# Kernel tuning notes

Hardware: AMD Instinct MI355X
Metric: run time of the kernel (lower is better)

Reference implementation:

```python
import jax, jax.numpy as jnp
import numpy as np

B, C, N, K = 8, 256, 1024, 16
CQ = C // 4
EPS_BN = 1e-5

def setup_inputs() -> dict:
    key = jax.random.key(0)
    ks = jax.random.split(key, 8)
    s = lambda fan: 1.0 / np.sqrt(fan)
    return {
        "x": jax.random.normal(ks[0], (B, C, N, K), dtype=jnp.float32),
        "q_w": jax.random.normal(ks[1], (CQ, C), dtype=jnp.float32) * s(C),
        "k_w": jax.random.normal(ks[2], (CQ, C), dtype=jnp.float32) * s(C),
        "v_w": jax.random.normal(ks[3], (C, C), dtype=jnp.float32) * s(C),
        "v_b": jax.random.normal(ks[4], (C,), dtype=jnp.float32) * 0.01,
        "t_w": jax.random.normal(ks[5], (C, C), dtype=jnp.float32) * s(C),
        "t_b": jax.random.normal(ks[6], (C,), dtype=jnp.float32) * 0.01,
        "gamma": jnp.ones((C,), dtype=jnp.float32),
        "beta": jnp.zeros((C,), dtype=jnp.float32),
    }

def reference(x, q_w, k_w, v_w, v_b, t_w, t_b, gamma, beta):
    # 1x1 convs == channel matmuls
    xq = jnp.einsum('bcnk,oc->bonk', x, q_w)                  # [B,CQ,N,K]
    xk = jnp.einsum('bcnk,oc->bonk', x, k_w)                  # [B,CQ,N,K]
    xv = jnp.einsum('bcnk,oc->bonk', x, v_w) + v_b[None, :, None, None]  # [B,C,N,K]
    x_q = jnp.transpose(xq, (0, 3, 2, 1))                     # [B,K,N,CQ]
    x_k = jnp.transpose(xk, (0, 3, 1, 2))                     # [B,K,CQ,N]
    x_v = jnp.transpose(xv, (0, 3, 1, 2))                     # [B,K,C,N]
    energy = jnp.einsum('bknd,bkdm->bknm', x_q, x_k)          # [B,K,N,N]
    attn = jax.nn.softmax(energy, axis=-1)
    # non-standard renormalization across the K (neighbourhood) axis
    attn = attn / (1e-9 + jnp.sum(attn, axis=1, keepdims=True))
    x_r = jnp.einsum('bkcn,bknm->bkcm', x_v, attn)            # [B,K,C,N]
    x_r = jnp.transpose(x_r, (0, 2, 3, 1))                    # [B,C,N,K]
    d = x - x_r
    t = jnp.einsum('bcnk,oc->bonk', d, t_w) + t_b[None, :, None, None]
    # BatchNorm2d (training-mode batch statistics, biased variance)
    mean = jnp.mean(t, axis=(0, 2, 3), keepdims=True)
    var = jnp.mean((t - mean) ** 2, axis=(0, 2, 3), keepdims=True)
    t_hat = (t - mean) / jnp.sqrt(var + EPS_BN)
    r = jax.nn.relu(t_hat * gamma[None, :, None, None] + beta[None, :, None, None])
    return x + r
```

## Files before the change

kernel.cpp:

```cpp
#include <hip/hip_runtime.h>
#include <hip/hip_bf16.h>
#include <cstdint>
#include <cstddef>

#define NB   8
#define NCHN 256
#define NSP  1024
#define NKK  16
#define NCQ  64
#define NPK  16384
#define NBK  128

typedef __hip_bfloat16 bf16;
typedef unsigned short u16;
typedef __attribute__((ext_vector_type(8))) short bf16x8;
typedef __attribute__((ext_vector_type(4))) float f32x4;

__device__ __forceinline__ float bf2f(bf16 v) { return __bfloat162float(v); }

__device__ __forceinline__ u16 f2bf(float x) {
  unsigned b = __float_as_uint(x);
  return (u16)((b + 0x7FFF + ((b >> 16) & 1)) >> 16);
}
__device__ __forceinline__ float bfr2f(u16 u) { return __uint_as_float(((unsigned)u) << 16); }

__device__ __forceinline__ void stage64(const u16* __restrict__ g, u16* __restrict__ l, int t) {
  #pragma unroll
  for (int i = 0; i < 2; ++i) {
    const int idx = t + i * 256;
    const int row = idx >> 3, col = (idx & 7) * 8;
    const bf16x8 v = *reinterpret_cast<const bf16x8*>(g + (size_t)row * 64 + col);
    *reinterpret_cast<bf16x8*>(l + row * 72 + col) = v;
  }
}

__global__ __launch_bounds__(256) void k_w2(const float* __restrict__ t_w,
                                            const float* __restrict__ v_w,
                                            const float* __restrict__ v_b,
                                            float* __restrict__ w2,
                                            float* __restrict__ ub) {
  const int o = blockIdx.x;
  const int c = threadIdx.x;
  __shared__ float trow[NCHN];
  __shared__ float red[NCHN];
  trow[c] = t_w[o * NCHN + c];
  __syncthreads();
  float acc = 0.f;
  for (int m = 0; m < NCHN; ++m) acc = fmaf(trow[m], v_w[m * NCHN + c], acc);
  w2[o * NCHN + c] = acc;
  red[c] = trow[c] * v_b[c];
  __syncthreads();
  for (int s = 128; s > 0; s >>= 1) {
    if (c < s) red[c] += red[c + s];
    __syncthreads();
  }
  if (c == 0) ub[o] = red[0];
}

__global__ __launch_bounds__(256) void k_wsplit(
    const float* __restrict__ q_w, const float* __restrict__ k_w,
    const float* __restrict__ w2, const float* __restrict__ t_w,
    u16* __restrict__ wh, u16* __restrict__ wl) {
  const int o = blockIdx.x, c = threadIdx.x;
  float v;
  if (o < 64)       v = q_w[o * NCHN + c];
  else if (o < 128) v = k_w[(o - 64) * NCHN + c];
  else if (o < 384) v = w2[(o - 128) * NCHN + c];
  else              v = t_w[(o - 384) * NCHN + c];
  const u16 hi = f2bf(v);
  wh[o * NCHN + c] = hi;
  wl[o * NCHN + c] = f2bf(v - bfr2f(hi));
}

__global__ __launch_bounds__(256) void k_xsplit(
    const float* __restrict__ x, u16* __restrict__ xh, u16* __restrict__ xl) {
  const int c0 = blockIdx.x * 64, p0 = blockIdx.y * 64, b = blockIdx.z;
  const int t = threadIdx.x;
  __shared__ float tile[64][65];
  const float* xb = x + ((size_t)b * NCHN + c0) * NPK + p0;
  #pragma unroll
  for (int it = 0; it < 4; ++it) {
    const int item = t + it * 256;
    const int row = item >> 4, colg = item & 15;
    const float4 v = *reinterpret_cast<const float4*>(xb + (size_t)row * NPK + colg * 4);
    tile[row][colg * 4 + 0] = v.x;
    tile[row][colg * 4 + 1] = v.y;
    tile[row][colg * 4 + 2] = v.z;
    tile[row][colg * 4 + 3] = v.w;
  }
  __syncthreads();
  #pragma unroll
  for (int it = 0; it < 2; ++it) {
    const int item = t + it * 256;
    const int pl = item >> 3, cg = item & 7;
    u16 hi[8], lo[8];
    #pragma unroll
    for (int jj = 0; jj < 8; ++jj) {
      const float v = tile[cg * 8 + jj][pl];
      hi[jj] = f2bf(v);
      lo[jj] = f2bf(v - bfr2f(hi[jj]));
    }
    const int p = p0 + pl;
    const int pp = (p & 15) * NSP + (p >> 4);
    const size_t base = ((size_t)b * NPK + pp) * NCHN + c0 + cg * 8;
    *reinterpret_cast<bf16x8*>(xh + base) = *reinterpret_cast<const bf16x8*>(hi);
    *reinterpret_cast<bf16x8*>(xl + base) = *reinterpret_cast<const bf16x8*>(lo);
  }
}

__global__ void k_zero(float* __restrict__ p, int n) {
  int i = blockIdx.x * 256 + threadIdx.x;
  if (i < n) p[i] = 0.f;
}

__global__ __launch_bounds__(256) void k_projm(
    const u16* __restrict__ xh, const u16* __restrict__ xl,
    const u16* __restrict__ wh, const u16* __restrict__ wl,
    const float* __restrict__ ub,
    u16* __restrict__ qh, u16* __restrict__ ql,
    u16* __restrict__ kh, u16* __restrict__ kl,
    u16* __restrict__ u, u16* __restrict__ s) {
  const int oh = blockIdx.x;
  const int p0 = blockIdx.y * 64;
  const int kk = p0 >> 10;
  const int n0 = p0 & 1023;
  const int b  = blockIdx.z;
  const int t = threadIdx.x, w = t >> 6, lane = t & 63, l15 = lane & 15, quad = lane >> 4;
  const int obase = oh * 320 + w * 80;
  const bool anyqk = obase < 128;
  __shared__ u16 lxh[64 * 264];
  __shared__ u16 lxl[64 * 264];
  const u16* xhb = xh + ((size_t)b * NPK + p0) * NCHN;
  const u16* xlb = xl + ((size_t)b * NPK + p0) * NCHN;
  #pragma unroll
  for (int i = 0; i < 8; ++i) {
    const int idx = t + i * 256;
    const int row = idx >> 5, col8 = (idx & 31) * 8;
    *reinterpret_cast<bf16x8*>(&lxh[row * 264 + col8]) =
        *reinterpret_cast<const bf16x8*>(xhb + (size_t)row * NCHN + col8);
  }
  if (oh == 0) {
    #pragma unroll
    for (int i = 0; i < 8; ++i) {
      const int idx = t + i * 256;
      const int row = idx >> 5, col8 = (idx & 31) * 8;
      *reinterpret_cast<bf16x8*>(&lxl[row * 264 + col8]) =
          *reinterpret_cast<const bf16x8*>(xlb + (size_t)row * NCHN + col8);
    }
  }
  __syncthreads();
  f32x4 acc[5][4] = {};
  for (int kc = 0; kc < 8; ++kc) {
    const int c0 = kc * 32 + quad * 8;
    bf16x8 bhf[4], blf[4];
    #pragma unroll
    for (int fj = 0; fj < 4; ++fj) {
      bhf[fj] = *reinterpret_cast<const bf16x8*>(&lxh[(fj * 16 + l15) * 264 + c0]);
      if (anyqk) blf[fj] = *reinterpret_cast<const bf16x8*>(&lxl[(fj * 16 + l15) * 264 + c0]);
    }
    #pragma unroll
    for (int fi = 0; fi < 5; ++fi) {
      const int orow = obase + fi * 16;
      const size_t aoff = (size_t)(orow + l15) * NCHN + c0;
      const bf16x8 ah = *reinterpret_cast<const bf16x8*>(wh + aoff);
      if (orow < 128) {
        const bf16x8 al = *reinterpret_cast<const bf16x8*>(wl + aoff);
        #pragma unroll
        for (int fj = 0; fj < 4; ++fj) {
          acc[fi][fj] = __builtin_amdgcn_mfma_f32_16x16x32_bf16(ah, bhf[fj], acc[fi][fj], 0, 0, 0);
          acc[fi][fj] = __builtin_amdgcn_mfma_f32_16x16x32_bf16(ah, blf[fj], acc[fi][fj], 0, 0, 0);
          acc[fi][fj] = __builtin_amdgcn_mfma_f32_16x16x32_bf16(al, bhf[fj], acc[fi][fj], 0, 0, 0);
        }
      } else {
        #pragma unroll
        for (int fj = 0; fj < 4; ++fj)
          acc[fi][fj] = __builtin_amdgcn_mfma_f32_16x16x32_bf16(bhf[fj], ah, acc[fi][fj], 0, 0, 0);
      }
    }
  }
  #pragma unroll
  for (int fi = 0; fi < 5; ++fi) {
    const int orow = obase + fi * 16;
    if (orow < 128) {
      const int ob = orow + quad * 4;
      #pragma unroll
      for (int fj = 0; fj < 4; ++fj) {
        const int n = n0 + fj * 16 + l15;
        ushort4 hv, lv;
        #pragma unroll
        for (int r = 0; r < 4; ++r) {
          const float v = acc[fi][fj][r];
          const u16 hi = f2bf(v);
          ((u16*)&hv)[r] = hi;
          ((u16*)&lv)[r] = f2bf(v - bfr2f(hi));
        }
        const size_t rowb = ((size_t)(b * NKK + kk) * NSP + n) * NCQ;
        if (ob < 64) {
          *reinterpret_cast<ushort4*>(qh + rowb + ob) = hv;
          *reinterpret_cast<ushort4*>(ql + rowb + ob) = lv;
        } else {
          *reinterpret_cast<ushort4*>(kh + rowb + (ob - 64)) = hv;
          *reinterpret_cast<ushort4*>(kl + rowb + (ob - 64)) = lv;
        }
      }
    } else if (orow < 384) {
      const int c = orow + l15 - 128;
      const float uc = ub[c];
      u16* up = u + ((size_t)(b * NKK + kk) * NCHN + c) * NSP;
      #pragma unroll
      for (int fj = 0; fj < 4; ++fj) {
        const int n = n0 + fj * 16 + quad * 4;
        ushort4 uv;
        #pragma unroll
        for (int r = 0; r < 4; ++r) ((u16*)&uv)[r] = f2bf(acc[fi][fj][r] + uc);
        *reinterpret_cast<ushort4*>(up + n) = uv;
      }
    } else {
      const int c = orow + l15 - 384;
      u16* sp = s + (((size_t)b * NCHN + c) * NKK + kk) * NSP;
      #pragma unroll
      for (int fj = 0; fj < 4; ++fj) {
        const int n = n0 + fj * 16 + quad * 4;
        ushort4 sv;
        #pragma unroll
        for (int r = 0; r < 4; ++r) ((u16*)&sv)[r] = f2bf(acc[fi][fj][r]);
        *reinterpret_cast<ushort4*>(sp + n) = sv;
      }
    }
  }
}

__global__ __launch_bounds__(256) void k_stats(
    const u16* __restrict__ qh_g, const u16* __restrict__ ql_g,
    const u16* __restrict__ kh_g, const u16* __restrict__ kl_g,
    float* __restrict__ m_i, float* __restrict__ inv_l) {
  const int n0 = blockIdx.x * 64;
  const int bk = blockIdx.y;
  const int t = threadIdx.x;
  const int w = t >> 6, lane = t & 63, l15 = lane & 15, quad = lane >> 4;
  __shared__ u16 sqh[64 * 72], sql[64 * 72], skh[64 * 72], skl[64 * 72];
  const size_t qoff = (size_t)bk * NSP * NCQ + (size_t)n0 * NCQ;
  stage64(qh_g + qoff, sqh, t);
  stage64(ql_g + qoff, sql, t);
  float runmax[4] = {-1e30f, -1e30f, -1e30f, -1e30f};
  float runsum[4] = {0.f, 0.f, 0.f, 0.f};
  const int arow = w * 16 + l15;
  for (int mt = 0; mt < 16; ++mt) {
    __syncthreads();
    const size_t koff = (size_t)bk * NSP * NCQ + (size_t)(mt * 64) * NCQ;
    stage64(kh_g + koff, skh, t);
    stage64(kl_g + koff, skl, t);
    __syncthreads();
    f32x4 e[4] = {};
    #pragma unroll
    for (int ks = 0; ks < 2; ++ks) {
      const bf16x8 ah = *(const bf16x8*)&sqh[arow * 72 + ks * 32 + quad * 8];
      const bf16x8 al = *(const bf16x8*)&sql[arow * 72 + ks * 32 + quad * 8];
      #pragma unroll
      for (int fj = 0; fj < 4; ++fj) {
        const int brow = fj * 16 + l15;
        const bf16x8 bh = *(const bf16x8*)&skh[brow * 72 + ks * 32 + quad * 8];
        const bf16x8 bl = *(const bf16x8*)&skl[brow * 72 + ks * 32 + quad * 8];
        e[fj] = __builtin_amdgcn_mfma_f32_16x16x32_bf16(ah, bh, e[fj], 0, 0, 0);
        e[fj] = __builtin_amdgcn_mfma_f32_16x16x32_bf16(ah, bl, e[fj], 0, 0, 0);
        e[fj] = __builtin_amdgcn_mfma_f32_16x16x32_bf16(al, bh, e[fj], 0, 0, 0);
      }
    }
    #pragma unroll
    for (int r = 0; r < 4; ++r) {
      float tmax = fmaxf(fmaxf(e[0][r], e[1][r]), fmaxf(e[2][r], e[3][r]));
      tmax = fmaxf(tmax, __shfl_xor(tmax, 1));
      tmax = fmaxf(tmax, __shfl_xor(tmax, 2));
      tmax = fmaxf(tmax, __shfl_xor(tmax, 4));
      tmax = fmaxf(tmax, __shfl_xor(tmax, 8));
      const float nm = fmaxf(runmax[r], tmax);
      float ts = __expf(e[0][r] - nm) + __expf(e[1][r] - nm) +
                 __expf(e[2][r] - nm) + __expf(e[3][r] - nm);
      ts += __shfl_xor(ts, 1);
      ts += __shfl_xor(ts, 2);
      ts += __shfl_xor(ts, 4);
      ts += __shfl_xor(ts, 8);
      runsum[r] = runsum[r] * __expf(runmax[r] - nm) + ts;
      runmax[r] = nm;
    }
  }
  if (l15 == 0) {
    #pragma unroll
    for (int r = 0; r < 4; ++r) {
      const int n = n0 + w * 16 + quad * 4 + r;
      m_i[(size_t)bk * NSP + n] = runmax[r];
      inv_l[(size_t)bk * NSP + n] = 1.0f / runsum[r];
    }
  }
}

__global__ __launch_bounds__(256) void k_denom(
    const u16* __restrict__ qh_g, const u16* __restrict__ ql_g,
    const u16* __restrict__ kh_g, const u16* __restrict__ kl_g,
    const float* __restrict__ m_i, const float* __restrict__ inv_l,
    float* __restrict__ invden) {
  const int m0 = blockIdx.x * 64, n0 = blockIdx.y * 64, b = blockIdx.z;
  const int t = threadIdx.x;
  const int w = t >> 6, lane = t & 63, l15 = lane & 15, quad = lane >> 4;
  __shared__ u16 sqh[64 * 72], sql[64 * 72], skh[64 * 72], skl[64 * 72];
  float den[4][4] = {};
  const int arow = w * 16 + l15;
  for (int kk = 0; kk < NKK; ++kk) {
    const int bk = b * NKK + kk;
    __syncthreads();
    const size_t qoff = (size_t)bk * NSP * NCQ + (size_t)n0 * NCQ;
    const size_t koff = (size_t)bk * NSP * NCQ + (size_t)m0 * NCQ;
    stage64(qh_g + qoff, sqh, t);
    stage64(ql_g + qoff, sql, t);
    stage64(kh_g + koff, skh, t);
    stage64(kl_g + koff, skl, t);
    __syncthreads();
    f32x4 e[4] = {};
    #pragma unroll
    for (int ks = 0; ks < 2; ++ks) {
      const bf16x8 ah = *(const bf16x8*)&sqh[arow * 72 + ks * 32 + quad * 8];
      const bf16x8 al = *(const bf16x8*)&sql[arow * 72 + ks * 32 + quad * 8];
      #pragma unroll
      for (int fj = 0; fj < 4; ++fj) {
        const int brow = fj * 16 + l15;
        const bf16x8 bh = *(const bf16x8*)&skh[brow * 72 + ks * 32 + quad * 8];
        const bf16x8 bl = *(const bf16x8*)&skl[brow * 72 + ks * 32 + quad * 8];
        e[fj] = __builtin_amdgcn_mfma_f32_16x16x32_bf16(ah, bh, e[fj], 0, 0, 0);
        e[fj] = __builtin_amdgcn_mfma_f32_16x16x32_bf16(ah, bl, e[fj], 0, 0, 0);
        e[fj] = __builtin_amdgcn_mfma_f32_16x16x32_bf16(al, bh, e[fj], 0, 0, 0);
      }
    }
    float smv[4], slv[4];
    #pragma unroll
    for (int r = 0; r < 4; ++r) {
      const int n = n0 + w * 16 + quad * 4 + r;
      smv[r] = m_i[(size_t)bk * NSP + n];
      slv[r] = inv_l[(size_t)bk * NSP + n];
    }
    #pragma unroll
    for (int fj = 0; fj < 4; ++fj)
      #pragma unroll
      for (int r = 0; r < 4; ++r)
        den[fj][r] += __expf(e[fj][r] - smv[r]) * slv[r];
  }
  #pragma unroll
  for (int fj = 0; fj < 4; ++fj)
    #pragma unroll
    for (int r = 0; r < 4; ++r) {
      const int n = n0 + w * 16 + quad * 4 + r;
      invden[(size_t)b * NSP * NSP + (size_t)n * NSP + m0 + fj * 16 + l15] =
          1.0f / (1e-9f + den[fj][r]);
    }
}

__global__ __launch_bounds__(256) void k_xr(
    const u16* __restrict__ qh_g, const u16* __restrict__ ql_g,
    const u16* __restrict__ kh_g, const u16* __restrict__ kl_g,
    const u16* __restrict__ u_g, const float* __restrict__ m_i,
    const float* __restrict__ inv_l, const float* __restrict__ invden,
    u16* __restrict__ txr) {
  const int m0 = blockIdx.x * 64;
  const int bk = blockIdx.y;
  const int b = bk >> 4;
  const int t = threadIdx.x;
  const int w = t >> 6, lane = t & 63, l15 = lane & 15, quad = lane >> 4;
  __shared__ u16 sqh[64 * 72], sql[64 * 72], skh[64 * 72], skl[64 * 72];
  __shared__ u16 sat[64 * 72];
  f32x4 acc[4][4] = {};
  const size_t koff = (size_t)bk * NSP * NCQ + (size_t)m0 * NCQ;
  stage64(kh_g + koff, skh, t);
  stage64(kl_g + koff, skl, t);
  const float* dp = invden + (size_t)b * NSP * NSP;
  const u16* up = u_g + (size_t)bk * NCHN * NSP;
  const int arow = w * 16 + l15;
  for (int nt = 0; nt < 16; ++nt) {
    const int n0 = nt * 64;
    __syncthreads();
    const size_t qoff = (size_t)bk * NSP * NCQ + (size_t)n0 * NCQ;
    stage64(qh_g + qoff, sqh, t);
    stage64(ql_g + qoff, sql, t);
    __syncthreads();
    f32x4 e[4] = {};
    #pragma unroll
    for (int ks = 0; ks < 2; ++ks) {
      const bf16x8 ah = *(const bf16x8*)&sqh[arow * 72 + ks * 32 + quad * 8];
      const bf16x8 al = *(const bf16x8*)&sql[arow * 72 + ks * 32 + quad * 8];
      #pragma unroll
      for (int fj = 0; fj < 4; ++fj) {
        const int brow = fj * 16 + l15;
        const bf16x8 bh = *(const bf16x8*)&skh[brow * 72 + ks * 32 + quad * 8];
        const bf16x8 bl = *(const bf16x8*)&skl[brow * 72 + ks * 32 + quad * 8];
        e[fj] = __builtin_amdgcn_mfma_f32_16x16x32_bf16(ah, bh, e[fj], 0, 0, 0);
        e[fj] = __builtin_amdgcn_mfma_f32_16x16x32_bf16(ah, bl, e[fj], 0, 0, 0);
        e[fj] = __builtin_amdgcn_mfma_f32_16x16x32_bf16(al, bh, e[fj], 0, 0, 0);
      }
    }
    float smv[4], slv[4];
    #pragma unroll
    for (int r = 0; r < 4; ++r) {
      const int n = n0 + w * 16 + quad * 4 + r;
      smv[r] = m_i[(size_t)bk * NSP + n];
      slv[r] = inv_l[(size_t)bk * NSP + n];
    }
    #pragma unroll
    for (int fj = 0; fj < 4; ++fj) {
      const int m = m0 + fj * 16 + l15;
      float p[4];
      #pragma unroll
      for (int r = 0; r < 4; ++r) {
        const int n = n0 + w * 16 + quad * 4 + r;
        p[r] = __expf(e[fj][r] - smv[r]) * slv[r] * dp[(size_t)n * NSP + m];
      }
      ushort4 pk;
      pk.x = f2bf(p[0]); pk.y = f2bf(p[1]); pk.z = f2bf(p[2]); pk.w = f2bf(p[3]);
      *reinterpret_cast<ushort4*>(&sat[(fj * 16 + l15) * 72 + w * 16 + quad * 4]) = pk;
    }
    __syncthreads();
    #pragma unroll
    for (int ks = 0; ks < 2; ++ks) {
      bf16x8 bfr[4];
      #pragma unroll
      for (int fj = 0; fj < 4; ++fj)
        bfr[fj] = *(const bf16x8*)&sat[(fj * 16 + l15) * 72 + ks * 32 + quad * 8];
      #pragma unroll
      for (int ci = 0; ci < 4; ++ci) {
        const int c = w * 64 + ci * 16 + l15;
        const bf16x8 a =
            *reinterpret_cast<const bf16x8*>(up + (size_t)c * NSP + n0 + ks * 32 + quad * 8);
        #pragma unroll
        for (int fj = 0; fj < 4; ++fj)
          acc[ci][fj] = __builtin_amdgcn_mfma_f32_16x16x32_bf16(a, bfr[fj], acc[ci][fj], 0, 0, 0);
      }
    }
  }
  #pragma unroll
  for (int ci = 0; ci < 4; ++ci)
    #pragma unroll
    for (int fj = 0; fj < 4; ++fj)
      #pragma unroll
      for (int r = 0; r < 4; ++r) {
        const int c = w * 64 + ci * 16 + quad * 4 + r;
        const int m = m0 + fj * 16 + l15;
        txr[((size_t)bk * NCHN + c) * NSP + m] = f2bf(acc[ci][fj][r]);
      }
}

__global__ __launch_bounds__(256) void k_bnstats(
    const u16* __restrict__ s, const u16* __restrict__ txr,
    const float* __restrict__ t_b, float* __restrict__ bnsum,
    float* __restrict__ bnsq) {
  const int c = blockIdx.x, b = blockIdx.y, t = threadIdx.x;
  __shared__ float r1[256], r2[256];
  const u16* sp = s + (size_t)(b * NCHN + c) * NKK * NSP;
  const u16* tp = txr + ((size_t)b * NKK * NCHN + c) * NSP;
  const float tb = t_b[c];
  float lsum = 0.f, lss = 0.f;
  #pragma unroll
  for (int it = 0; it < 8; ++it) {
    const int idx = (it * 256 + t) * 8;
    const int kk = idx >> 10, n = idx & 1023;
    const bf16x8 s8 = *reinterpret_cast<const bf16x8*>(sp + idx);
    const bf16x8 t8 = *reinterpret_cast<const bf16x8*>(tp + (size_t)kk * NCHN * NSP + n);
    #pragma unroll
    for (int j = 0; j < 8; ++j) {
      const float tv = bfr2f((u16)s8[j]) + tb - bfr2f((u16)t8[j]);
      lsum += tv;
      lss = fmaf(tv, tv, lss);
    }
  }
  r1[t] = lsum; r2[t] = lss;
  __syncthreads();
  for (int sh = 128; sh > 0; sh >>= 1) {
    if (t < sh) { r1[t] += r1[t + sh]; r2[t] += r2[t + sh]; }
    __syncthreads();
  }
  if (t == 0) {
    atomicAdd(&bnsum[c], r1[0]);
    atomicAdd(&bnsq[c], r2[0]);
  }
}

__global__ void k_bnfin(const float* __restrict__ bnsum, const float* __restrict__ bnsq,
                        const float* __restrict__ gamma, const float* __restrict__ beta,
                        float* __restrict__ abuf, float* __restrict__ bbuf) {
  const int c = threadIdx.x;
  const float inv_m = 1.0f / 131072.0f;
  const float mean = bnsum[c] * inv_m;
  const float var = bnsq[c] * inv_m - mean * mean;
  const float a = gamma[c] * rsqrtf(var + 1e-5f);
  abuf[c] = a;
  bbuf[c] = beta[c] - mean * a;
}

__global__ __launch_bounds__(256) void k_out(
    const float* __restrict__ x, const u16* __restrict__ s,
    const u16* __restrict__ txr, const float* __restrict__ t_b,
    const float* __restrict__ abuf, const float* __restrict__ bbuf,
    float* __restrict__ out) {
  const int c = blockIdx.x, b = blockIdx.y, t = threadIdx.x;
  __shared__ u16 txl[16 * 264];
  __shared__ u16 sxl[16 * 264];
  const u16* sp = s + (size_t)(b * NCHN + c) * NKK * NSP;
  const u16* tp = txr + ((size_t)b * NKK * NCHN + c) * NSP;
  const float* xp = x + ((size_t)b * NCHN + c) * NPK;
  float* op = out + ((size_t)b * NCHN + c) * NPK;
  const float tb = t_b[c], a = abuf[c], bb = bbuf[c];
  for (int n0 = 0; n0 < NSP; n0 += 256) {
    __syncthreads();
    #pragma unroll
    for (int it = 0; it < 2; ++it) {
      const int item = it * 256 + t;
      const int kk = item >> 5, nn8 = (item & 31) * 8;
      *reinterpret_cast<bf16x8*>(&txl[kk * 264 + nn8]) =
          *reinterpret_cast<const bf16x8*>(tp + (size_t)kk * NCHN * NSP + n0 + nn8);
      *reinterpret_cast<bf16x8*>(&sxl[kk * 264 + nn8]) =
          *reinterpret_cast<const bf16x8*>(sp + (size_t)kk * NSP + n0 + nn8);
    }
    __syncthreads();
    for (int i2 = t; i2 < 1024; i2 += 256) {
      const int idx = i2 * 4;
      const int nn = idx >> 4, k0 = idx & 15;
      const float4 xv = *reinterpret_cast<const float4*>(xp + (size_t)n0 * NKK + idx);
      float4 ov;
      float* ovp = &ov.x;
      const float* xvp = &xv.x;
      #pragma unroll
      for (int j = 0; j < 4; ++j) {
        const int kk = k0 + j;
        const float tv = bfr2f(sxl[kk * 264 + nn]) + tb - bfr2f(txl[kk * 264 + nn]);
        ovp[j] = xvp[j] + fmaxf(fmaf(tv, a, bb), 0.f);
      }
      *reinterpret_cast<float4*>(op + (size_t)n0 * NKK + idx) = ov;
    }
  }
}

extern "C" void kernel_launch(void* const* d_in, const int* in_sizes, int n_in,
                              void* d_out, int out_size, void* d_ws, size_t ws_size,
                              hipStream_t stream) {
  (void)in_sizes; (void)n_in; (void)out_size; (void)ws_size;
  const float* x     = (const float*)d_in[0];
  const float* q_w   = (const float*)d_in[1];
  const float* k_w   = (const float*)d_in[2];
  const float* v_w   = (const float*)d_in[3];
  const float* v_b   = (const float*)d_in[4];
  const float* t_w   = (const float*)d_in[5];
  const float* t_b   = (const float*)d_in[6];
  const float* gamma = (const float*)d_in[7];
  const float* beta  = (const float*)d_in[8];
  float* out = (float*)d_out;

  char* w = (char*)d_ws;
  float* invden = (float*)w; w += (size_t)NB * NSP * NSP * 4;
  u16*   txr    = (u16*)w;   w += (size_t)NBK * NCHN * NSP * 2;
  u16*   qh     = (u16*)w;   w += (size_t)NBK * NSP * NCQ * 2;
  u16*   ql     = (u16*)w;   w += (size_t)NBK * NSP * NCQ * 2;
  u16*   kh     = (u16*)w;   w += (size_t)NBK * NSP * NCQ * 2;
  u16*   kl     = (u16*)w;   w += (size_t)NBK * NSP * NCQ * 2;
  u16*   u      = (u16*)w;   w += (size_t)NBK * NCHN * NSP * 2;
  u16*   s      = (u16*)w;   w += (size_t)NB * NCHN * NPK * 2;
  u16*   xh     = (u16*)w;   w += (size_t)NB * NPK * NCHN * 2;
  u16*   xl     = (u16*)w;   w += (size_t)NB * NPK * NCHN * 2;
  u16*   whb    = (u16*)w;   w += (size_t)640 * NCHN * 2;
  u16*   wlb    = (u16*)w;   w += (size_t)640 * NCHN * 2;
  float* m_i    = (float*)w; w += (size_t)NBK * NSP * 4;
  float* inv_l  = (float*)w; w += (size_t)NBK * NSP * 4;
  float* w2     = (float*)w; w += (size_t)NCHN * NCHN * 4;
  float* ub     = (float*)w; w += 1024;
  float* bnsum  = (float*)w; w += 1024;
  float* bnsq   = (float*)w; w += 1024;
  float* abuf   = (float*)w; w += 1024;
  float* bbuf   = (float*)w; w += 1024;

  k_zero<<<dim3(2), dim3(256), 0, stream>>>(bnsum, 512);
  k_w2<<<dim3(256), dim3(256), 0, stream>>>(t_w, v_w, v_b, w2, ub);
  k_wsplit<<<dim3(640), dim3(256), 0, stream>>>(q_w, k_w, w2, t_w, whb, wlb);
  k_xsplit<<<dim3(4, 256, NB), dim3(256), 0, stream>>>(x, xh, xl);
  k_projm<<<dim3(2, 256, NB), dim3(256), 0, stream>>>(xh, xl, whb, wlb, ub,
                                                      qh, ql, kh, kl, u, s);
  k_stats<<<dim3(16, NBK), dim3(256), 0, stream>>>(qh, ql, kh, kl, m_i, inv_l);
  k_denom<<<dim3(16, 16, NB), dim3(256), 0, stream>>>(qh, ql, kh, kl, m_i, inv_l, invden);
  k_xr<<<dim3(16, NBK), dim3(256), 0, stream>>>(qh, ql, kh, kl, u, m_i,
                                                inv_l, invden, txr);
  k_bnstats<<<dim3(NCHN, NB), dim3(256), 0, stream>>>(s, txr, t_b, bnsum, bnsq);
  k_bnfin<<<dim3(1), dim3(256), 0, stream>>>(bnsum, bnsq, gamma, beta, abuf, bbuf);
  k_out<<<dim3(NCHN, NB), dim3(256), 0, stream>>>(x, s, txr, t_b, abuf, bbuf, out);
}
```

Baseline: 1.006 ms.

## Materialize energy matrix once and reuse it in denominator and xr kernels

The stats kernel now writes the fp32 energy matrix to a scratch buffer that reuses the xh workspace. The denominator and xr kernels read it back instead of recomputing QK^T with three split-bf16 MFMAs each. The work is processed in four chunks of 32 (batch, neighbour) slices so the energy buffer fits in the existing workspace, and the denominator becomes a simple elementwise reduction over the K axis. This removes two of the three energy recomputations but adds a large amount of fp32 global traffic, 128 MB per chunk written and read twice, plus more kernel launches.

Measured after the change: 1.517 ms. 1.51x slower.

```diff
diff --git a/kernel.cpp b/kernel.cpp
--- a/kernel.cpp
+++ b/kernel.cpp
@@ -233,9 +233,11 @@
 __global__ __launch_bounds__(256) void k_stats(
     const u16* __restrict__ qh_g, const u16* __restrict__ ql_g,
     const u16* __restrict__ kh_g, const u16* __restrict__ kl_g,
-    float* __restrict__ m_i, float* __restrict__ inv_l) {
-  const int n0 = blockIdx.x * 64;
-  const int bk = blockIdx.y;
+    float* __restrict__ m_i, float* __restrict__ inv_l,
+    float* __restrict__ eng, int bk0) {
+  const int bkl = blockIdx.x;
+  const int n0 = blockIdx.y * 64;
+  const int bk = bk0 + bkl;
   const int t = threadIdx.x;
   const int w = t >> 6, lane = t & 63, l15 = lane & 15, quad = lane >> 4;
   __shared__ u16 sqh[64 * 72], sql[64 * 72], skh[64 * 72], skl[64 * 72];
@@ -245,6 +247,7 @@
   float runmax[4] = {-1e30f, -1e30f, -1e30f, -1e30f};
   float runsum[4] = {0.f, 0.f, 0.f, 0.f};
   const int arow = w * 16 + l15;
+  float* ep = eng + (size_t)bkl * NSP * NSP;
   for (int mt = 0; mt < 16; ++mt) {
     __syncthreads();
     const size_t koff = (size_t)bk * NSP * NCQ + (size_t)(mt * 64) * NCQ;
@@ -265,6 +268,11 @@
         e[fj] = __builtin_amdgcn_mfma_f32_16x16x32_bf16(ah, bl, e[fj], 0, 0, 0);
         e[fj] = __builtin_amdgcn_mfma_f32_16x16x32_bf16(al, bh, e[fj], 0, 0, 0);
       }
+    }
+    #pragma unroll
+    for (int fj = 0; fj < 4; ++fj) {
+      const int m = mt * 64 + fj * 16 + l15;
+      *reinterpret_cast<f32x4*>(ep + (size_t)m * NSP + n0 + w * 16 + quad * 4) = e[fj];
     }
     #pragma unroll
     for (int r = 0; r < 4; ++r) {
@@ -294,134 +302,81 @@
   }
 }
 
-__global__ __launch_bounds__(256) void k_denom(
-    const u16* __restrict__ qh_g, const u16* __restrict__ ql_g,
-    const u16* __restrict__ kh_g, const u16* __restrict__ kl_g,
-    const float* __restrict__ m_i, const float* __restrict__ inv_l,
-    float* __restrict__ invden) {
-  const int m0 = blockIdx.x * 64, n0 = blockIdx.y * 64, b = blockIdx.z;
+__global__ __launch_bounds__(256) void k_denl(
+    const float* __restrict__ eng, const float* __restrict__ m_i,
+    const float* __restrict__ inv_l, float* __restrict__ invden, int bk0) {
+  const int m = blockIdx.x;
+  const int bl = blockIdx.y;
   const int t = threadIdx.x;
-  const int w = t >> 6, lane = t & 63, l15 = lane & 15, quad = lane >> 4;
-  __shared__ u16 sqh[64 * 72], sql[64 * 72], skh[64 * 72], skl[64 * 72];
-  float den[4][4] = {};
-  const int arow = w * 16 + l15;
+  const int n4 = t * 4;
+  const int b = (bk0 >> 4) + bl;
+  f32x4 acc = {0.f, 0.f, 0.f, 0.f};
   for (int kk = 0; kk < NKK; ++kk) {
-    const int bk = b * NKK + kk;
-    __syncthreads();
-    const size_t qoff = (size_t)bk * NSP * NCQ + (size_t)n0 * NCQ;
-    const size_t koff = (size_t)bk * NSP * NCQ + (size_t)m0 * NCQ;
-    stage64(qh_g + qoff, sqh, t);
-    stage64(ql_g + qoff, sql, t);
-    stage64(kh_g + koff, skh, t);
-    stage64(kl_g + koff, skl, t);
-    __syncthreads();
-    f32x4 e[4] = {};
-    #pragma unroll
-    for (int ks = 0; ks < 2; ++ks) {
-      const bf16x8 ah = *(const bf16x8*)&sqh[arow * 72 + ks * 32 + quad * 8];
-      const bf16x8 al = *(const bf16x8*)&sql[arow * 72 + ks * 32 + quad * 8];
-      #pragma unroll
-      for (int fj = 0; fj < 4; ++fj) {
-        const int brow = fj * 16 + l15;
-        const bf16x8 bh = *(const bf16x8*)&skh[brow * 72 + ks * 32 + quad * 8];
-        const bf16x8 bl = *(const bf16x8*)&skl[brow * 72 + ks * 32 + quad * 8];
-        e[fj] = __builtin_amdgcn_mfma_f32_16x16x32_bf16(ah, bh, e[fj], 0, 0, 0);
-        e[fj] = __builtin_amdgcn_mfma_f32_16x16x32_bf16(ah, bl, e[fj], 0, 0, 0);
-        e[fj] = __builtin_amdgcn_mfma_f32_16x16x32_bf16(al, bh, e[fj], 0, 0, 0);
-      }
-    }
-    float smv[4], slv[4];
-    #pragma unroll
-    for (int r = 0; r < 4; ++r) {
-      const int n = n0 + w * 16 + quad * 4 + r;
-      smv[r] = m_i[(size_t)bk * NSP + n];
-      slv[r] = inv_l[(size_t)bk * NSP + n];
-    }
-    #pragma unroll
-    for (int fj = 0; fj < 4; ++fj)
-      #pragma unroll
-      for (int r = 0; r < 4; ++r)
-        den[fj][r] += __expf(e[fj][r] - smv[r]) * slv[r];
-  }
-  #pragma unroll
-  for (int fj = 0; fj < 4; ++fj)
-    #pragma unroll
-    for (int r = 0; r < 4; ++r) {
-      const int n = n0 + w * 16 + quad * 4 + r;
-      invden[(size_t)b * NSP * NSP + (size_t)n * NSP + m0 + fj * 16 + l15] =
-          1.0f / (1e-9f + den[fj][r]);
-    }
+    const int bkl = bl * 16 + kk;
+    const int bk = bk0 + bkl;
+    const f32x4 e4 = *reinterpret_cast<const f32x4*>(eng + ((size_t)bkl * NSP + m) * NSP + n4);
+    const f32x4 mi = *reinterpret_cast<const f32x4*>(m_i + (size_t)bk * NSP + n4);
+    const f32x4 il = *reinterpret_cast<const f32x4*>(inv_l + (size_t)bk * NSP + n4);
+    #pragma unroll
+    for (int j = 0; j < 4; ++j) acc[j] = fmaf(__expf(e4[j] - mi[j]), il[j], acc[j]);
+  }
+  f32x4 o;
+  #pragma unroll
+  for (int j = 0; j < 4; ++j) o[j] = 1.0f / (1e-9f + acc[j]);
+  *reinterpret_cast<f32x4*>(invden + ((size_t)b * NSP + m) * NSP + n4) = o;
 }
 
 __global__ __launch_bounds__(256) void k_xr(
-    const u16* __restrict__ qh_g, const u16* __restrict__ ql_g,
-    const u16* __restrict__ kh_g, const u16* __restrict__ kl_g,
-    const u16* __restrict__ u_g, const float* __restrict__ m_i,
+    const float* __restrict__ eng, const float* __restrict__ m_i,
     const float* __restrict__ inv_l, const float* __restrict__ invden,
-    u16* __restrict__ txr) {
-  const int m0 = blockIdx.x * 64;
-  const int bk = blockIdx.y;
+    const u16* __restrict__ u_g, u16* __restrict__ txr, int bk0) {
+  const int bkl = blockIdx.x;
+  const int m0 = blockIdx.y * 64;
+  const int bk = bk0 + bkl;
   const int b = bk >> 4;
   const int t = threadIdx.x;
   const int w = t >> 6, lane = t & 63, l15 = lane & 15, quad = lane >> 4;
-  __shared__ u16 sqh[64 * 72], sql[64 * 72], skh[64 * 72], skl[64 * 72];
-  __shared__ u16 sat[64 * 72];
-  f32x4 acc[4][4] = {};
-  const size_t koff = (size_t)bk * NSP * NCQ + (size_t)m0 * NCQ;
-  stage64(kh_g + koff, skh, t);
-  stage64(kl_g + koff, skl, t);
+  __shared__ float sil[NSP];
+  __shared__ float smx[NSP];
+  #pragma unroll
+  for (int i = 0; i < 4; ++i) {
+    sil[t + i * 256] = inv_l[(size_t)bk * NSP + t + i * 256];
+    smx[t + i * 256] = m_i[(size_t)bk * NSP + t + i * 256];
+  }
+  __syncthreads();
+  const float* ep = eng + (size_t)bkl * NSP * NSP;
   const float* dp = invden + (size_t)b * NSP * NSP;
   const u16* up = u_g + (size_t)bk * NCHN * NSP;
-  const int arow = w * 16 + l15;
+  f32x4 acc[4][4] = {};
   for (int nt = 0; nt < 16; ++nt) {
     const int n0 = nt * 64;
-    __syncthreads();
-    const size_t qoff = (size_t)bk * NSP * NCQ + (size_t)n0 * NCQ;
-    stage64(qh_g + qoff, sqh, t);
-    stage64(ql_g + qoff, sql, t);
-    __syncthreads();
-    f32x4 e[4] = {};
+    bf16x8 pb[2][4];
     #pragma unroll
     for (int ks = 0; ks < 2; ++ks) {
-      const bf16x8 ah = *(const bf16x8*)&sqh[arow * 72 + ks * 32 + quad * 8];
-      const bf16x8 al = *(const bf16x8*)&sql[arow * 72 + ks * 32 + quad * 8];
+      const int nb = n0 + ks * 32 + quad * 8;
+      const f32x4 il0 = *reinterpret_cast<const f32x4*>(&sil[nb]);
+      const f32x4 il1 = *reinterpret_cast<const f32x4*>(&sil[nb + 4]);
+      const f32x4 mx0 = *reinterpret_cast<const f32x4*>(&smx[nb]);
+      const f32x4 mx1 = *reinterpret_cast<const f32x4*>(&smx[nb + 4]);
       #pragma unroll
       for (int fj = 0; fj < 4; ++fj) {
-        const int brow = fj * 16 + l15;
-        const bf16x8 bh = *(const bf16x8*)&skh[brow * 72 + ks * 32 + quad * 8];
-        const bf16x8 bl = *(const bf16x8*)&skl[brow * 72 + ks * 32 + quad * 8];
-        e[fj] = __builtin_amdgcn_mfma_f32_16x16x32_bf16(ah, bh, e[fj], 0, 0, 0);
-        e[fj] = __builtin_amdgcn_mfma_f32_16x16x32_bf16(ah, bl, e[fj], 0, 0, 0);
-        e[fj] = __builtin_amdgcn_mfma_f32_16x16x32_bf16(al, bh, e[fj], 0, 0, 0);
-      }
-    }
-    float smv[4], slv[4];
-    #pragma unroll
-    for (int r = 0; r < 4; ++r) {
-      const int n = n0 + w * 16 + quad * 4 + r;
-      smv[r] = m_i[(size_t)bk * NSP + n];
-      slv[r] = inv_l[(size_t)bk * NSP + n];
-    }
-    #pragma unroll
-    for (int fj = 0; fj < 4; ++fj) {
-      const int m = m0 + fj * 16 + l15;
-      float p[4];
-      #pragma unroll
-      for (int r = 0; r < 4; ++r) {
-        const int n = n0 + w * 16 + quad * 4 + r;
-        p[r] = __expf(e[fj][r] - smv[r]) * slv[r] * dp[(size_t)n * NSP + m];
-      }
-      ushort4 pk;
-      pk.x = f2bf(p[0]); pk.y = f2bf(p[1]); pk.z = f2bf(p[2]); pk.w = f2bf(p[3]);
-      *reinterpret_cast<ushort4*>(&sat[(fj * 16 + l15) * 72 + w * 16 + quad * 4]) = pk;
-    }
-    __syncthreads();
-    #pragma unroll
-    for (int ks = 0; ks < 2; ++ks) {
-      bf16x8 bfr[4];
-      #pragma unroll
-      for (int fj = 0; fj < 4; ++fj)
-        bfr[fj] = *(const bf16x8*)&sat[(fj * 16 + l15) * 72 + ks * 32 + quad * 8];
+        const size_t roff = (size_t)(m0 + fj * 16 + l15) * NSP + nb;
+        const f32x4 e0 = *reinterpret_cast<const f32x4*>(ep + roff);
+        const f32x4 e1 = *reinterpret_cast<const f32x4*>(ep + roff + 4);
+        const f32x4 d0 = *reinterpret_cast<const f32x4*>(dp + roff);
+        const f32x4 d1 = *reinterpret_cast<const f32x4*>(dp + roff + 4);
+        u16 o[8];
+        #pragma unroll
+        for (int j = 0; j < 4; ++j)
+          o[j] = f2bf(__expf(e0[j] - mx0[j]) * il0[j] * d0[j]);
+        #pragma unroll
+        for (int j = 0; j < 4; ++j)
+          o[j + 4] = f2bf(__expf(e1[j] - mx1[j]) * il1[j] * d1[j]);
+        pb[ks][fj] = *reinterpret_cast<const bf16x8*>(o);
+      }
+    }
+    #pragma unroll
+    for (int ks = 0; ks < 2; ++ks)
       #pragma unroll
       for (int ci = 0; ci < 4; ++ci) {
         const int c = w * 64 + ci * 16 + l15;
@@ -429,9 +384,8 @@
             *reinterpret_cast<const bf16x8*>(up + (size_t)c * NSP + n0 + ks * 32 + quad * 8);
         #pragma unroll
         for (int fj = 0; fj < 4; ++fj)
-          acc[ci][fj] = __builtin_amdgcn_mfma_f32_16x16x32_bf16(a, bfr[fj], acc[ci][fj], 0, 0, 0);
-      }
-    }
+          acc[ci][fj] = __builtin_amdgcn_mfma_f32_16x16x32_bf16(a, pb[ks][fj], acc[ci][fj], 0, 0, 0);
+      }
   }
   #pragma unroll
   for (int ci = 0; ci < 4; ++ci)
@@ -572,16 +526,20 @@
   float* abuf   = (float*)w; w += 1024;
   float* bbuf   = (float*)w; w += 1024;
 
+  float* eng = (float*)xh;
+
   k_zero<<<dim3(2), dim3(256), 0, stream>>>(bnsum, 512);
   k_w2<<<dim3(256), dim3(256), 0, stream>>>(t_w, v_w, v_b, w2, ub);
   k_wsplit<<<dim3(640), dim3(256), 0, stream>>>(q_w, k_w, w2, t_w, whb, wlb);
   k_xsplit<<<dim3(4, 256, NB), dim3(256), 0, stream>>>(x, xh, xl);
   k_projm<<<dim3(2, 256, NB), dim3(256), 0, stream>>>(xh, xl, whb, wlb, ub,
                                                       qh, ql, kh, kl, u, s);
-  k_stats<<<dim3(16, NBK), dim3(256), 0, stream>>>(qh, ql, kh, kl, m_i, inv_l);
-  k_denom<<<dim3(16, 16, NB), dim3(256), 0, stream>>>(qh, ql, kh, kl, m_i, inv_l, invden);
-  k_xr<<<dim3(16, NBK), dim3(256), 0, stream>>>(qh, ql, kh, kl, u, m_i,
-                                                inv_l, invden, txr);
+  for (int h = 0; h < 4; ++h) {
+    const int bk0 = h * 32;
+    k_stats<<<dim3(32, 16), dim3(256), 0, stream>>>(qh, ql, kh, kl, m_i, inv_l, eng, bk0);
+    k_denl<<<dim3(1024, 2), dim3(256), 0, stream>>>(eng, m_i, inv_l, invden, bk0);
+    k_xr<<<dim3(32, 16), dim3(256), 0, stream>>>(eng, m_i, inv_l, invden, u, txr, bk0);
+  }
   k_bnstats<<<dim3(NCHN, NB), dim3(256), 0, stream>>>(s, txr, t_b, bnsum, bnsq);
   k_bnfin<<<dim3(1), dim3(256), 0, stream>>>(bnsum, bnsq, gamma, beta, abuf, bbuf);
   k_out<<<dim3(NCHN, NB), dim3(256), 0, stream>>>(x, s, txr, t_b, abuf, bbuf, out);
```
